# Optimization experiments

Hardware: AMD Instinct MI355X
Metric: run time of the kernel (lower is better)

## Reference

```python
import jax, jax.numpy as jnp
import numpy as np

EPS = 1e-5

def _layernorm(x, g, b):
    mu = jnp.mean(x, axis=-1, keepdims=True)
    var = jnp.mean((x - mu) ** 2, axis=-1, keepdims=True)
    return (x - mu) / jnp.sqrt(var + EPS) * g + b


def setup_inputs() -> dict:
    key = jax.random.key(0)
    ks = jax.random.split(key, 4)
    B, H, W, C = 8, 96, 96, 256
    return {
        "x1": jax.random.normal(ks[0], (B, H, W, C), dtype=jnp.float32),
        "x2": jax.random.normal(ks[1], (B, H, W, C), dtype=jnp.float32),
        # norm1 (shared LayerNorm applied to both x1 and x2)
        "g1": jnp.ones((C,), jnp.float32),
        "b1": jnp.zeros((C,), jnp.float32),
        # reprojection 1x1 conv: C -> 2C
        "Wr": jax.random.normal(ks[2], (2 * C, C), dtype=jnp.float32) * 0.05,
        "br": jnp.zeros((2 * C,), jnp.float32),
        # final LayerNorm over 2C
        "g2": jnp.ones((2 * C,), jnp.float32),
        "b2": jnp.zeros((2 * C,), jnp.float32),
        # learnable mixing scalars
        "a1": jnp.array(0.25, jnp.float32),
        "a2": jnp.array(0.25, jnp.float32),
        "a3": jnp.array(0.25, jnp.float32),
        "a4": jnp.array(0.25, jnpp_ := jnp.float32),
    }


def reference(x1, x2, g1, b1, Wr, br, g2, b2, a1, a2, a3, a4):
    B, H, W, C = x1.shape
    N, D = H * W, C  # head_count = 1, key_channels = value_channels = D
    n1 = _layernorm(x1.reshape(B, N, C), g1, b1)  # [B,N,D]
    n2 = _layernorm(x2.reshape(B, N, C), g1, b1)

    kq = jnp.swapaxes(n2, 1, 2)                   # [B,D,N]
    key_sm = jax.nn.softmax(kq, axis=2)           # softmax over N
    query = jax.nn.softmax(kq, axis=1)            # softmax over D
    value = jnp.swapaxes(n1, 1, 2)                # [B,D,N]

    # context = key @ value^T : [B,D,D]
    context = jnp.einsum('bdn,ben->bde', key_sm, value)

    def masked_softmax(k):
        # torch.topk + scatter mask == keep entries >= k-th largest per row
        thr = jax.lax.top_k(context, k)[0][..., -1:]
        return jax.nn.softmax(jnp.where(context >= thr, context, -jnp.inf), axis=-1)

    ks = [D // 2, (D * 2) // 3, (D * 3) // 4, (D * 4) // 5]
    o = [jnp.einsum('bde,ben->bdn', masked_softmax(k), query) for k in ks]
    att = a1 * o[0] + a2 * o[1] + a3 * o[2] + a4 * o[3]  # [B,D,N]

    # 1x1 conv reprojection D -> 2D, then LayerNorm over channels
    rep = jnp.einsum('oc,bcn->bno', Wr, att) + br         # [B,N,2D]
    rep = _layernorm(rep, g2, b2)
    # view(B,H,W,2C).permute(0,3,1,2)
    return jnp.transpose(rep.reshape(B, H, W, 2 * C), (0, 3, 1, 2))
```

## Files before the change

### kernel.cpp

```cpp
#include <hip/hip_runtime.h>
#include <hip/hip_bf16.h>

#define Bc 8
#define Nn 9216
#define Dd 256
#define Oo 512
#define EPSc 1e-5f

#define OFF_MU1    0
#define OFF_RSTD1  73728
#define OFF_MU2    147456
#define OFF_RSTD2  221184
#define OFF_ROWINV 294912
#define OFF_COLSUM 368640
#define OFF_M      894976
#define OFF_W2T    1419264
#define OFF_CTXP   2467840

typedef __attribute__((ext_vector_type(4))) float f32x4;
typedef __attribute__((ext_vector_type(8))) short short8;
typedef __attribute__((ext_vector_type(8))) unsigned short ushort8;

static __device__ __forceinline__ unsigned short f2bf(float f) {
    __hip_bfloat16 h = __float2bfloat16(f);
    union { __hip_bfloat16 hh; unsigned short uu; } cv; cv.hh = h;
    return cv.uu;
}

#define SWZ(ch) (((((ch) >> 2) & 7)) ^ ((((ch) & 3)) << 1))

__global__ __launch_bounds__(256) void mg_k0_zero(float* __restrict__ p, int n4) {
    int i = blockIdx.x * 256 + threadIdx.x;
    if (i < n4) ((float4*)p)[i] = make_float4(0.f, 0.f, 0.f, 0.f);
}

__global__ __launch_bounds__(256) void mg_k1_stats(const float* __restrict__ x1, const float* __restrict__ x2,
                                                   const float* __restrict__ g1, const float* __restrict__ b1,
                                                   float* __restrict__ ws)
{
    float* mu1    = ws + OFF_MU1;
    float* rstd1  = ws + OFF_RSTD1;
    float* mu2    = ws + OFF_MU2;
    float* rstd2  = ws + OFF_RSTD2;
    float* rowinv = ws + OFF_ROWINV;
    float* colsum = ws + OFF_COLSUM;

    int t = threadIdx.x, lane = t & 63, w = t >> 6;
    int b = blockIdx.x / 144, rb = blockIdx.x % 144;
    int nbase = rb * 64;

    float4 g1v = ((const float4*)g1)[lane];
    float4 b1v = ((const float4*)b1)[lane];
    float cs0 = 0.f, cs1 = 0.f, cs2 = 0.f, cs3 = 0.f;
    __shared__ float csL[4][256];

    for (int i = 0; i < 16; ++i) {
        int n = nbase + i * 4 + w;
        int base = (b * Nn + n) * 64 + lane;
        float4 xa = ((const float4*)x1)[base];
        float4 xb = ((const float4*)x2)[base];
        float s1 = xa.x + xa.y + xa.z + xa.w;
        float q1 = xa.x*xa.x + xa.y*xa.y + xa.z*xa.z + xa.w*xa.w;
        float s2 = xb.x + xb.y + xb.z + xb.w;
        float q2 = xb.x*xb.x + xb.y*xb.y + xb.z*xb.z + xb.w*xb.w;
        #pragma unroll
        for (int m = 1; m < 64; m <<= 1) {
            s1 += __shfl_xor(s1, m); q1 += __shfl_xor(q1, m);
            s2 += __shfl_xor(s2, m); q2 += __shfl_xor(q2, m);
        }
        float m1 = s1 * (1.f / Dd), m2 = s2 * (1.f / Dd);
        float r1 = rsqrtf(q1 * (1.f / Dd) - m1 * m1 + EPSc);
        float r2 = rsqrtf(q2 * (1.f / Dd) - m2 * m2 + EPSc);
        int ni = b * Nn + n;
        if (lane == 0) { mu1[ni] = m1; rstd1[ni] = r1; mu2[ni] = m2; rstd2[ni] = r2; }
        float e0 = __expf((xb.x - m2) * r2 * g1v.x + b1v.x);
        float e1 = __expf((xb.y - m2) * r2 * g1v.y + b1v.y);
        float e2 = __expf((xb.z - m2) * r2 * g1v.z + b1v.z);
        float e3 = __expf((xb.w - m2) * r2 * g1v.w + b1v.w);
        float rs = e0 + e1 + e2 + e3;
        #pragma unroll
        for (int m = 1; m < 64; m <<= 1) rs += __shfl_xor(rs, m);
        if (lane == 0) rowinv[ni] = 1.f / rs;
        cs0 += e0; cs1 += e1; cs2 += e2; cs3 += e3;
    }
    csL[w][lane * 4 + 0] = cs0;
    csL[w][lane * 4 + 1] = cs1;
    csL[w][lane * 4 + 2] = cs2;
    csL[w][lane * 4 + 3] = cs3;
    __syncthreads();
    float tot = csL[0][t] + csL[1][t] + csL[2][t] + csL[3][t];
    atomicAdd(&colsum[b * Dd + t], tot);
}

__global__ __launch_bounds__(512, 2) void mg_k3_ctx(const float* __restrict__ x1, const float* __restrict__ x2,
                                                    const float* __restrict__ g1, const float* __restrict__ b1,
                                                    float* __restrict__ ws, int nks)
{
    __shared__ ushort PA[256 * 64];
    __shared__ ushort PB[256 * 64];
    const float* mu1   = ws + OFF_MU1;
    const float* rstd1 = ws + OFF_RSTD1;
    const float* mu2   = ws + OFF_MU2;
    const float* rstd2 = ws + OFF_RSTD2;
    float* ctxp = ws + OFF_CTXP;

    int t = threadIdx.x;
    int ks_i = blockIdx.x % nks;
    int b = blockIdx.x / nks;
    int krange = Nn / nks;
    int ntiles = krange >> 6;
    int n_base = ks_i * krange;

    int o  = t >> 6;
    int c4 = t & 63;

    f32x4 g1v = ((const f32x4*)g1)[c4];
    f32x4 b1v = ((const f32x4*)b1)[c4];

    int lane = t & 63, wave = t >> 6;
    int wd = wave & 3, we = wave >> 2;
    int l15 = lane & 15, kgrp = lane >> 4;

    f32x4 acc[4][8];
    #pragma unroll
    for (int dt = 0; dt < 4; ++dt)
        #pragma unroll
        for (int et = 0; et < 8; ++et) acc[dt][et] = (f32x4){0.f, 0.f, 0.f, 0.f};

    for (int st = 0; st < ntiles; ++st) {
        int rowb = b * Nn + n_base + st * 64 + o * 8;
        __syncthreads();
        {
            f32x4 mv0 = *(const f32x4*)(mu1 + rowb),   mv1 = *(const f32x4*)(mu1 + rowb + 4);
            f32x4 rv0 = *(const f32x4*)(rstd1 + rowb), rv1 = *(const f32x4*)(rstd1 + rowb + 4);
            float mva[8] = {mv0[0], mv0[1], mv0[2], mv0[3], mv1[0], mv1[1], mv1[2], mv1[3]};
            float rva[8] = {rv0[0], rv0[1], rv0[2], rv0[3], rv1[0], rv1[1], rv1[2], rv1[3]};
            f32x4 xv[8];
            #pragma unroll
            for (int rr = 0; rr < 8; ++rr)
                xv[rr] = ((const f32x4*)x1)[(size_t)(rowb + rr) * 64 + c4];
            #pragma unroll
            for (int i = 0; i < 4; ++i) {
                int ch = c4 * 4 + i;
                ushort8 u;
                #pragma unroll
                for (int rr = 0; rr < 8; ++rr)
                    u[rr] = f2bf((xv[rr][i] - mva[rr]) * rva[rr] * g1v[i] + b1v[i]);
                *(ushort8*)&PB[ch * 64 + ((o + SWZ(ch)) & 7) * 8] = u;
            }
        }
        {
            f32x4 mv0 = *(const f32x4*)(mu2 + rowb),   mv1 = *(const f32x4*)(mu2 + rowb + 4);
            f32x4 rv0 = *(const f32x4*)(rstd2 + rowb), rv1 = *(const f32x4*)(rstd2 + rowb + 4);
            float mva[8] = {mv0[0], mv0[1], mv0[2], mv0[3], mv1[0], mv1[1], mv1[2], mv1[3]};
            float rva[8] = {rv0[0], rv0[1], rv0[2], rv0[3], rv1[0], rv1[1], rv1[2], rv1[3]};
            f32x4 xv[8];
            #pragma unroll
            for (int rr = 0; rr < 8; ++rr)
                xv[rr] = ((const f32x4*)x2)[(size_t)(rowb + rr) * 64 + c4];
            #pragma unroll
            for (int i = 0; i < 4; ++i) {
                int ch = c4 * 4 + i;
                ushort8 u;
                #pragma unroll
                for (int rr = 0; rr < 8; ++rr)
                    u[rr] = f2bf(__expf((xv[rr][i] - mva[rr]) * rva[rr] * g1v[i] + b1v[i]));
                *(ushort8*)&PA[ch * 64 + ((o + SWZ(ch)) & 7) * 8] = u;
            }
        }
        __syncthreads();

        #pragma unroll
        for (int kk = 0; kk < 2; ++kk) {
            short8 af[4], bf[8];
            #pragma unroll
            for (int dt = 0; dt < 4; ++dt) {
                int ch = wd * 64 + dt * 16 + l15;
                af[dt] = *(const short8*)&PA[ch * 64 + (((kk << 2) + kgrp + SWZ(ch)) & 7) * 8];
            }
            #pragma unroll
            for (int et = 0; et < 8; ++et) {
                int ch = we * 128 + et * 16 + l15;
                bf[et] = *(const short8*)&PB[ch * 64 + (((kk << 2) + kgrp + SWZ(ch)) & 7) * 8];
            }
            #pragma unroll
            for (int dt = 0; dt < 4; ++dt)
                #pragma unroll
                for (int et = 0; et < 8; ++et)
                    acc[dt][et] = __builtin_amdgcn_mfma_f32_16x16x32_bf16(af[dt], bf[et], acc[dt][et], 0, 0, 0);
        }
    }

    size_t obase = ((size_t)ks_i * Bc + b) * (Dd * Dd);
    #pragma unroll
    for (int dt = 0; dt < 4; ++dt) {
        #pragma unroll
        for (int r = 0; r < 4; ++r) {
            int d = wd * 64 + dt * 16 + kgrp * 4 + r;
            float* rowp = ctxp + obase + (size_t)d * Dd + we * 128 + l15;
            #pragma unroll
            for (int et = 0; et < 8; ++et)
                rowp[et * 16] = acc[dt][et][r];
        }
    }
}

__global__ __launch_bounds__(256) void mg_k5_mask(const float* __restrict__ a1p, const float* __restrict__ a2p,
                                                  const float* __restrict__ a3p, const float* __restrict__ a4p,
                                                  float* __restrict__ ws, int nks)
{
    const float* ctxp   = ws + OFF_CTXP;
    const float* colsum = ws + OFF_COLSUM;
    float* Mo = ws + OFF_M;
    int t = threadIdx.x;
    int b = blockIdx.x >> 8, d = blockIdx.x & 255;
    __shared__ float s[256];
    __shared__ float wred[4][4];

    float c = 0.f;
    for (int p = 0; p < nks; ++p)
        c += ctxp[((size_t)p * Bc + b) * (Dd * Dd) + (size_t)d * Dd + t];
    float inv = 1.f / colsum[b * Dd + d];
    c *= inv;
    s[t] = c;
    __syncthreads();
    for (int k = 2; k <= 256; k <<= 1) {
        for (int j = k >> 1; j > 0; j >>= 1) {
            int ixj = t ^ j;
            if (ixj > t) {
                float A = s[t], Bv = s[ixj];
                bool desc = ((t & k) == 0);
                bool sw = desc ? (A < Bv) : (A > Bv);
                if (sw) { s[t] = Bv; s[ixj] = A; }
            }
            __syncthreads();
        }
    }
    float cmax = s[0];
    float t0 = s[127], t1 = s[169], t2 = s[191], t3 = s[203];
    float e = __expf(c - cmax);
    float w0 = (c >= t0) ? e : 0.f;
    float w1 = (c >= t1) ? e : 0.f;
    float w2 = (c >= t2) ? e : 0.f;
    float w3 = (c >= t3) ? e : 0.f;
    float v0 = w0, v1 = w1, v2 = w2, v3 = w3;
    #pragma unroll
    for (int m = 1; m < 64; m <<= 1) {
        v0 += __shfl_xor(v0, m); v1 += __shfl_xor(v1, m);
        v2 += __shfl_xor(v2, m); v3 += __shfl_xor(v3, m);
    }
    int lane = t & 63, wv = t >> 6;
    if (lane == 0) { wred[wv][0] = v0; wred[wv][1] = v1; wred[wv][2] = v2; wred[wv][3] = v3; }
    __syncthreads();
    float S0 = wred[0][0] + wred[1][0] + wred[2][0] + wred[3][0];
    float S1 = wred[0][1] + wred[1][1] + wred[2][1] + wred[3][1];
    float S2 = wred[0][2] + wred[1][2] + wred[2][2] + wred[3][2];
    float S3 = wred[0][3] + wred[1][3] + wred[2][3] + wred[3][3];
    float Mv = a1p[0] * (w0 / S0) + a2p[0] * (w1 / S1) + a3p[0] * (w2 / S2) + a4p[0] * (w3 / S3);
    Mo[(b * Dd + d) * Dd + t] = Mv;
}

__global__ __launch_bounds__(256) void mg_k6_w2(const float* __restrict__ Wr, float* __restrict__ ws)
{
    const float* Mo = ws + OFF_M;
    ushort* W2B = (ushort*)(ws + OFF_W2T);
    __shared__ float Mt[32][128];
    __shared__ float WrT[32][36];
    int t = threadIdx.x;
    int b = blockIdx.x >> 5, ob = (blockIdx.x >> 1) & 15, eh = blockIdx.x & 1;
    int o0 = ob * 32, e0 = eh * 128;
    int ol4 = t & 7, el = t >> 3;
    float acc[4][4];
    #pragma unroll
    for (int i = 0; i < 4; ++i)
        #pragma unroll
        for (int j = 0; j < 4; ++j) acc[i][j] = 0.f;

    for (int ch = 0; ch < 8; ++ch) {
        int c0 = ch * 32;
        __syncthreads();
        #pragma unroll
        for (int k = 0; k < 4; ++k) {
            int fi = t + k * 256;
            int row = fi >> 5, c4 = fi & 31;
            float4 mv = ((const float4*)Mo)[(b * Dd + c0 + row) * 64 + (e0 >> 2) + c4];
            *(float4*)&Mt[row][c4 * 4] = mv;
        }
        {
            int ol = t >> 3, c4 = t & 7;
            float4 wv = ((const float4*)Wr)[(o0 + ol) * 64 + (c0 >> 2) + c4];
            WrT[c4 * 4 + 0][ol] = wv.x;
            WrT[c4 * 4 + 1][ol] = wv.y;
            WrT[c4 * 4 + 2][ol] = wv.z;
            WrT[c4 * 4 + 3][ol] = wv.w;
        }
        __syncthreads();
        #pragma unroll
        for (int cc = 0; cc < 32; ++cc) {
            float4 w4 = *(const float4*)&WrT[cc][ol4 * 4];
            float4 m4 = *(const float4*)&Mt[cc][el * 4];
            float wv[4] = {w4.x, w4.y, w4.z, w4.w};
            float mv[4] = {m4.x, m4.y, m4.z, m4.w};
            #pragma unroll
            for (int i = 0; i < 4; ++i)
                #pragma unroll
                for (int j = 0; j < 4; ++j)
                    acc[i][j] = fmaf(wv[i], mv[j], acc[i][j]);
        }
    }
    {
        int ee = e0 + el * 4;
        int ks = ee >> 5, eloc = ee & 31;
        #pragma unroll
        for (int i = 0; i < 4; ++i) {
            int o = o0 + ol4 * 4 + i;
            ushort4 u;
            u.x = f2bf(acc[i][0]); u.y = f2bf(acc[i][1]);
            u.z = f2bf(acc[i][2]); u.w = f2bf(acc[i][3]);
            *(ushort4*)&W2B[(((size_t)b * 8 + ks) * Oo + o) * 32 + eloc] = u;
        }
    }
}

__global__ __launch_bounds__(512) void mg_k7_final(const float* __restrict__ x2,
        const float* __restrict__ g1, const float* __restrict__ b1,
        const float* __restrict__ br, const float* __restrict__ g2, const float* __restrict__ b2,
        const float* __restrict__ ws, float* __restrict__ out)
{
    __shared__ ushort qsT[32 * 256];
    __shared__ float stat[8][2][16][2];
    __shared__ float musig[32][2];

    const float* mu2    = ws + OFF_MU2;
    const float* rstd2  = ws + OFF_RSTD2;
    const float* rowinv = ws + OFF_ROWINV;
    const ushort* W2B   = (const ushort*)(ws + OFF_W2T);

    int t = threadIdx.x;
    int b = blockIdx.x / 288, nt0 = blockIdx.x % 288;
    int n0 = nt0 * 32;

    {
        int row = t >> 4, gb = (t & 15) * 2;
        int ni = b * Nn + n0 + row;
        float m = mu2[ni], r = rstd2[ni], ri = rowinv[ni];
        #pragma unroll
        for (int jj = 0; jj < 2; ++jj) {
            int g = gb + jj;
            const float4* xp = (const float4*)x2 + (size_t)ni * 64 + g * 2;
            float4 xa = xp[0], xb = xp[1];
            float4 ga = ((const float4*)g1)[g * 2], gc = ((const float4*)g1)[g * 2 + 1];
            float4 ba = ((const float4*)b1)[g * 2], bc = ((const float4*)b1)[g * 2 + 1];
            float v[8]  = {xa.x, xa.y, xa.z, xa.w, xb.x, xb.y, xb.z, xb.w};
            float gv[8] = {ga.x, ga.y, ga.z, ga.w, gc.x, gc.y, gc.z, gc.w};
            float bv[8] = {ba.x, ba.y, ba.z, ba.w, bc.x, bc.y, bc.z, bc.w};
            ushort8 u;
            #pragma unroll
            for (int q = 0; q < 8; ++q)
                u[q] = f2bf(__expf((v[q] - m) * r * gv[q] + bv[q]) * ri);
            *(ushort8*)&qsT[row * 256 + ((g ^ (row & 7)) << 3)] = u;
        }
    }
    __syncthreads();

    int lw = t & 63, wave = t >> 6;
    int colA = lw & 15, kgrp = lw >> 4;

    f32x4 acc[4][2];
    #pragma unroll
    for (int ot = 0; ot < 4; ++ot) {
        acc[ot][0] = (f32x4){0.f, 0.f, 0.f, 0.f};
        acc[ot][1] = (f32x4){0.f, 0.f, 0.f, 0.f};
    }

    const ushort* abase = W2B + ((size_t)b * 8 * Oo + wave * 64 + colA) * 32 + kgrp * 8;

#define LOADAF(dst, ksv)                                                         \
    {                                                                            \
        _Pragma("unroll")                                                        \
        for (int ot = 0; ot < 4; ++ot)                                           \
            dst[ot] = *(const short8*)&abase[((size_t)(ksv) * Oo + ot * 16) * 32];\
    }

#define MFMASTEP(afv, ksv)                                                       \
    {                                                                            \
        int gsl = (((ksv) * 4 + kgrp) ^ (colA & 7)) << 3;                        \
        short8 bf0 = *(const short8*)&qsT[colA * 256 + gsl];                     \
        short8 bf1 = *(const short8*)&qsT[(16 + colA) * 256 + gsl];              \
        _Pragma("unroll")                                                        \
        for (int ot = 0; ot < 4; ++ot) {                                         \
            acc[ot][0] = __builtin_amdgcn_mfma_f32_16x16x32_bf16(                \
                afv[ot], bf0, acc[ot][0], 0, 0, 0);                              \
            acc[ot][1] = __builtin_amdgcn_mfma_f32_16x16x32_bf16(                \
                afv[ot], bf1, acc[ot][1], 0, 0, 0);                              \
        }                                                                        \
    }

    short8 afA[4], afB[4];
    LOADAF(afA, 0);
    #pragma unroll
    for (int kp = 0; kp < 4; ++kp) {
        LOADAF(afB, 2 * kp + 1);
        MFMASTEP(afA, 2 * kp);
        if (kp < 3) LOADAF(afA, 2 * kp + 2);
        MFMASTEP(afB, 2 * kp + 1);
    }
#undef LOADAF
#undef MFMASTEP

    float ps[2] = {0.f, 0.f}, pq[2] = {0.f, 0.f};
    #pragma unroll
    for (int ot = 0; ot < 4; ++ot) {
        #pragma unroll
        for (int r = 0; r < 4; ++r) {
            int o = wave * 64 + ot * 16 + kgrp * 4 + r;
            float bb = br[o];
            float v0 = acc[ot][0][r] + bb;
            float v1 = acc[ot][1][r] + bb;
            acc[ot][0][r] = v0; acc[ot][1][r] = v1;
            ps[0] += v0; pq[0] += v0 * v0;
            ps[1] += v1; pq[1] += v1 * v1;
        }
    }
    #pragma unroll
    for (int m = 16; m <= 32; m <<= 1) {
        ps[0] += __shfl_xor(ps[0], m); pq[0] += __shfl_xor(pq[0], m);
        ps[1] += __shfl_xor(ps[1], m); pq[1] += __shfl_xor(pq[1], m);
    }
    if (lw < 16) {
        stat[wave][0][lw][0] = ps[0]; stat[wave][0][lw][1] = pq[0];
        stat[wave][1][lw][0] = ps[1]; stat[wave][1][lw][1] = pq[1];
    }
    __syncthreads();
    if (t < 32) {
        int ntl = t >> 4, col = t & 15;
        float S = 0.f, Q = 0.f;
        #pragma unroll
        for (int w2 = 0; w2 < 8; ++w2) { S += stat[w2][ntl][col][0]; Q += stat[w2][ntl][col][1]; }
        float mu = S * (1.f / Oo);
        float var = Q * (1.f / Oo) - mu * mu;
        musig[t][0] = mu;
        musig[t][1] = rsqrtf(var + EPSc);
    }
    __syncthreads();

    float mn0 = musig[colA][0],      rs0 = musig[colA][1];
    float mn1 = musig[16 + colA][0], rs1 = musig[16 + colA][1];
    #pragma unroll
    for (int ot = 0; ot < 4; ++ot) {
        #pragma unroll
        for (int r = 0; r < 4; ++r) {
            int o = wave * 64 + ot * 16 + kgrp * 4 + r;
            float gg = g2[o], bb2 = b2[o];
            size_t ob = ((size_t)b * Oo + o) * Nn + n0;
            out[ob + colA]      = (acc[ot][0][r] - mn0) * rs0 * gg + bb2;
            out[ob + 16 + colA] = (acc[ot][1][r] - mn1) * rs1 * gg + bb2;
        }
    }
}

extern "C" void kernel_launch(void* const* d_in, const int* in_sizes, int n_in,
                              void* d_out, int out_size, void* d_ws, size_t ws_size,
                              hipStream_t stream)
{
    (void)in_sizes; (void)n_in; (void)out_size;
    const float* x1 = (const float*)d_in[0];
    const float* x2 = (const float*)d_in[1];
    const float* g1 = (const float*)d_in[2];
    const float* b1 = (const float*)d_in[3];
    const float* Wr = (const float*)d_in[4];
    const float* br = (const float*)d_in[5];
    const float* g2 = (const float*)d_in[6];
    const float* b2 = (const float*)d_in[7];
    const float* a1 = (const float*)d_in[8];
    const float* a2 = (const float*)d_in[9];
    const float* a3 = (const float*)d_in[10];
    const float* a4 = (const float*)d_in[11];
    float* ws = (float*)d_ws;
    float* out = (float*)d_out;

    const int cand[6] = {24, 16, 12, 8, 4, 2};
    int nks = 2;
    for (int ci = 0; ci < 6; ++ci) {
        if ((2467840ull + (size_t)cand[ci] * 524288ull) * 4ull <= ws_size) { nks = cand[ci]; break; }
    }

    hipLaunchKernelGGL(mg_k0_zero, dim3(2), dim3(256), 0, stream, ws + OFF_COLSUM, 512);
    hipLaunchKernelGGL(mg_k1_stats, dim3(1152), dim3(256), 0, stream, x1, x2, g1, b1, ws);
    hipLaunchKernelGGL(mg_k3_ctx, dim3(Bc * nks), dim3(512), 0, stream, x1, x2, g1, b1, ws, nks);
    hipLaunchKernelGGL(mg_k5_mask, dim3(2048), dim3(256), 0, stream, a1, a2, a3, a4, ws, nks);
    hipLaunchKernelGGL(mg_k6_w2, dim3(256), dim3(256), 0, stream, Wr, ws);
    hipLaunchKernelGGL(mg_k7_final, dim3(2304), dim3(512), 0, stream, x2, g1, b1, br, g2, b2, ws, out);
}
```

Before: 200.9 us.

## Fuse LayerNorm stats into the context kernel and cache bf16 query softmax

Drops the separate stats kernel. The context kernel now computes per-row LayerNorm mean and rstd, the row softmax sums and the column-sum partials itself, using wave shuffles and then an LDS reduction with an atomic add. That kernel also writes the softmax-over-D query as bf16 into a workspace buffer. The final kernel reads that buffer instead of reloading x2 and recomputing the exponentials. This removes a full extra pass over x1 and x2, and the fp32 re-read of x2, at the cost of more shuffle and exp work inside the small-grid context kernel and a larger workspace that may lower the chosen split count.

```diff
diff --git a/kernel.cpp b/kernel.cpp
--- a/kernel.cpp
+++ b/kernel.cpp
@@ -7,15 +7,11 @@
 #define Oo 512
 #define EPSc 1e-5f
 
-#define OFF_MU1    0
-#define OFF_RSTD1  73728
-#define OFF_MU2    147456
-#define OFF_RSTD2  221184
-#define OFF_ROWINV 294912
-#define OFF_COLSUM 368640
-#define OFF_M      894976
-#define OFF_W2T    1419264
-#define OFF_CTXP   2467840
+#define OFF_COLSUM 0
+#define OFF_M      2048
+#define OFF_W2T    526336
+#define OFF_QB     1050624
+#define OFF_CTXP   10487808
 
 typedef __attribute__((ext_vector_type(4))) float f32x4;
 typedef __attribute__((ext_vector_type(8))) short short8;
@@ -32,64 +28,6 @@
 __global__ __launch_bounds__(256) void mg_k0_zero(float* __restrict__ p, int n4) {
     int i = blockIdx.x * 256 + threadIdx.x;
     if (i < n4) ((float4*)p)[i] = make_float4(0.f, 0.f, 0.f, 0.f);
-}
-
-__global__ __launch_bounds__(256) void mg_k1_stats(const float* __restrict__ x1, const float* __restrict__ x2,
-                                                   const float* __restrict__ g1, const float* __restrict__ b1,
-                                                   float* __restrict__ ws)
-{
-    float* mu1    = ws + OFF_MU1;
-    float* rstd1  = ws + OFF_RSTD1;
-    float* mu2    = ws + OFF_MU2;
-    float* rstd2  = ws + OFF_RSTD2;
-    float* rowinv = ws + OFF_ROWINV;
-    float* colsum = ws + OFF_COLSUM;
-
-    int t = threadIdx.x, lane = t & 63, w = t >> 6;
-    int b = blockIdx.x / 144, rb = blockIdx.x % 144;
-    int nbase = rb * 64;
-
-    float4 g1v = ((const float4*)g1)[lane];
-    float4 b1v = ((const float4*)b1)[lane];
-    float cs0 = 0.f, cs1 = 0.f, cs2 = 0.f, cs3 = 0.f;
-    __shared__ float csL[4][256];
-
-    for (int i = 0; i < 16; ++i) {
-        int n = nbase + i * 4 + w;
-        int base = (b * Nn + n) * 64 + lane;
-        float4 xa = ((const float4*)x1)[base];
-        float4 xb = ((const float4*)x2)[base];
-        float s1 = xa.x + xa.y + xa.z + xa.w;
-        float q1 = xa.x*xa.x + xa.y*xa.y + xa.z*xa.z + xa.w*xa.w;
-        float s2 = xb.x + xb.y + xb.z + xb.w;
-        float q2 = xb.x*xb.x + xb.y*xb.y + xb.z*xb.z + xb.w*xb.w;
-        #pragma unroll
-        for (int m = 1; m < 64; m <<= 1) {
-            s1 += __shfl_xor(s1, m); q1 += __shfl_xor(q1, m);
-            s2 += __shfl_xor(s2, m); q2 += __shfl_xor(q2, m);
-        }
-        float m1 = s1 * (1.f / Dd), m2 = s2 * (1.f / Dd);
-        float r1 = rsqrtf(q1 * (1.f / Dd) - m1 * m1 + EPSc);
-        float r2 = rsqrtf(q2 * (1.f / Dd) - m2 * m2 + EPSc);
-        int ni = b * Nn + n;
-        if (lane == 0) { mu1[ni] = m1; rstd1[ni] = r1; mu2[ni] = m2; rstd2[ni] = r2; }
-        float e0 = __expf((xb.x - m2) * r2 * g1v.x + b1v.x);
-        float e1 = __expf((xb.y - m2) * r2 * g1v.y + b1v.y);
-        float e2 = __expf((xb.z - m2) * r2 * g1v.z + b1v.z);
-        float e3 = __expf((xb.w - m2) * r2 * g1v.w + b1v.w);
-        float rs = e0 + e1 + e2 + e3;
-        #pragma unroll
-        for (int m = 1; m < 64; m <<= 1) rs += __shfl_xor(rs, m);
-        if (lane == 0) rowinv[ni] = 1.f / rs;
-        cs0 += e0; cs1 += e1; cs2 += e2; cs3 += e3;
-    }
-    csL[w][lane * 4 + 0] = cs0;
-    csL[w][lane * 4 + 1] = cs1;
-    csL[w][lane * 4 + 2] = cs2;
-    csL[w][lane * 4 + 3] = cs3;
-    __syncthreads();
-    float tot = csL[0][t] + csL[1][t] + csL[2][t] + csL[3][t];
-    atomicAdd(&colsum[b * Dd + t], tot);
 }
 
 __global__ __launch_bounds__(512, 2) void mg_k3_ctx(const float* __restrict__ x1, const float* __restrict__ x2,
@@ -98,10 +36,9 @@
 {
     __shared__ ushort PA[256 * 64];
     __shared__ ushort PB[256 * 64];
-    const float* mu1   = ws + OFF_MU1;
-    const float* rstd1 = ws + OFF_RSTD1;
-    const float* mu2   = ws + OFF_MU2;
-    const float* rstd2 = ws + OFF_RSTD2;
+    __shared__ float csL[8][256];
+    float* colsum = ws + OFF_COLSUM;
+    ushort* qb = (ushort*)(ws + OFF_QB);
     float* ctxp = ws + OFF_CTXP;
 
     int t = threadIdx.x;
@@ -121,6 +58,8 @@
     int wd = wave & 3, we = wave >> 2;
     int l15 = lane & 15, kgrp = lane >> 4;
 
+    float cs[4] = {0.f, 0.f, 0.f, 0.f};
+
     f32x4 acc[4][8];
     #pragma unroll
     for (int dt = 0; dt < 4; ++dt)
@@ -131,14 +70,31 @@
         int rowb = b * Nn + n_base + st * 64 + o * 8;
         __syncthreads();
         {
-            f32x4 mv0 = *(const f32x4*)(mu1 + rowb),   mv1 = *(const f32x4*)(mu1 + rowb + 4);
-            f32x4 rv0 = *(const f32x4*)(rstd1 + rowb), rv1 = *(const f32x4*)(rstd1 + rowb + 4);
-            float mva[8] = {mv0[0], mv0[1], mv0[2], mv0[3], mv1[0], mv1[1], mv1[2], mv1[3]};
-            float rva[8] = {rv0[0], rv0[1], rv0[2], rv0[3], rv1[0], rv1[1], rv1[2], rv1[3]};
             f32x4 xv[8];
             #pragma unroll
             for (int rr = 0; rr < 8; ++rr)
                 xv[rr] = ((const f32x4*)x1)[(size_t)(rowb + rr) * 64 + c4];
+            float sA[8], qA[8];
+            #pragma unroll
+            for (int rr = 0; rr < 8; ++rr) {
+                f32x4 v = xv[rr];
+                sA[rr] = v[0] + v[1] + v[2] + v[3];
+                qA[rr] = v[0]*v[0] + v[1]*v[1] + v[2]*v[2] + v[3]*v[3];
+            }
+            #pragma unroll
+            for (int m = 1; m < 64; m <<= 1)
+                #pragma unroll
+                for (int rr = 0; rr < 8; ++rr) {
+                    sA[rr] += __shfl_xor(sA[rr], m);
+                    qA[rr] += __shfl_xor(qA[rr], m);
+                }
+            float mva[8], rva[8];
+            #pragma unroll
+            for (int rr = 0; rr < 8; ++rr) {
+                float mu = sA[rr] * (1.f / Dd);
+                mva[rr] = mu;
+                rva[rr] = rsqrtf(qA[rr] * (1.f / Dd) - mu * mu + EPSc);
+            }
             #pragma unroll
             for (int i = 0; i < 4; ++i) {
                 int ch = c4 * 4 + i;
@@ -150,22 +106,66 @@
             }
         }
         {
-            f32x4 mv0 = *(const f32x4*)(mu2 + rowb),   mv1 = *(const f32x4*)(mu2 + rowb + 4);
-            f32x4 rv0 = *(const f32x4*)(rstd2 + rowb), rv1 = *(const f32x4*)(rstd2 + rowb + 4);
-            float mva[8] = {mv0[0], mv0[1], mv0[2], mv0[3], mv1[0], mv1[1], mv1[2], mv1[3]};
-            float rva[8] = {rv0[0], rv0[1], rv0[2], rv0[3], rv1[0], rv1[1], rv1[2], rv1[3]};
             f32x4 xv[8];
             #pragma unroll
             for (int rr = 0; rr < 8; ++rr)
                 xv[rr] = ((const f32x4*)x2)[(size_t)(rowb + rr) * 64 + c4];
+            float sA[8], qA[8];
+            #pragma unroll
+            for (int rr = 0; rr < 8; ++rr) {
+                f32x4 v = xv[rr];
+                sA[rr] = v[0] + v[1] + v[2] + v[3];
+                qA[rr] = v[0]*v[0] + v[1]*v[1] + v[2]*v[2] + v[3]*v[3];
+            }
+            #pragma unroll
+            for (int m = 1; m < 64; m <<= 1)
+                #pragma unroll
+                for (int rr = 0; rr < 8; ++rr) {
+                    sA[rr] += __shfl_xor(sA[rr], m);
+                    qA[rr] += __shfl_xor(qA[rr], m);
+                }
+            float mva[8], rva[8];
+            #pragma unroll
+            for (int rr = 0; rr < 8; ++rr) {
+                float mu = sA[rr] * (1.f / Dd);
+                mva[rr] = mu;
+                rva[rr] = rsqrtf(qA[rr] * (1.f / Dd) - mu * mu + EPSc);
+            }
+            float ev[4][8];
+            #pragma unroll
+            for (int i = 0; i < 4; ++i)
+                #pragma unroll
+                for (int rr = 0; rr < 8; ++rr)
+                    ev[i][rr] = __expf((xv[rr][i] - mva[rr]) * rva[rr] * g1v[i] + b1v[i]);
+            float rsum[8];
+            #pragma unroll
+            for (int rr = 0; rr < 8; ++rr)
+                rsum[rr] = ev[0][rr] + ev[1][rr] + ev[2][rr] + ev[3][rr];
+            #pragma unroll
+            for (int m = 1; m < 64; m <<= 1)
+                #pragma unroll
+                for (int rr = 0; rr < 8; ++rr)
+                    rsum[rr] += __shfl_xor(rsum[rr], m);
             #pragma unroll
             for (int i = 0; i < 4; ++i) {
                 int ch = c4 * 4 + i;
                 ushort8 u;
                 #pragma unroll
-                for (int rr = 0; rr < 8; ++rr)
-                    u[rr] = f2bf(__expf((xv[rr][i] - mva[rr]) * rva[rr] * g1v[i] + b1v[i]));
+                for (int rr = 0; rr < 8; ++rr) {
+                    u[rr] = f2bf(ev[i][rr]);
+                    cs[i] += ev[i][rr];
+                }
                 *(ushort8*)&PA[ch * 64 + ((o + SWZ(ch)) & 7) * 8] = u;
+            }
+            #pragma unroll
+            for (int rr = 0; rr < 8; ++rr) {
+                float ri = 1.f / rsum[rr];
+                ushort4 uq;
+                uq.x = f2bf(ev[0][rr] * ri);
+                uq.y = f2bf(ev[1][rr] * ri);
+                uq.z = f2bf(ev[2][rr] * ri);
+                uq.w = f2bf(ev[3][rr] * ri);
+                *(ushort4*)&qb[(size_t)(rowb + rr) * 256 + c4 * 4] = uq;
             }
         }
         __syncthreads();
@@ -189,6 +189,16 @@
                 for (int et = 0; et < 8; ++et)
                     acc[dt][et] = __builtin_amdgcn_mfma_f32_16x16x32_bf16(af[dt], bf[et], acc[dt][et], 0, 0, 0);
         }
+    }
+
+    #pragma unroll
+    for (int i = 0; i < 4; ++i) csL[wave][c4 * 4 + i] = cs[i];
+    __syncthreads();
+    if (t < 256) {
+        float s = 0.f;
+        #pragma unroll
+        for (int w2 = 0; w2 < 8; ++w2) s += csL[w2][t];
+        atomicAdd(&colsum[b * Dd + t], s);
     }
 
     size_t obase = ((size_t)ks_i * Bc + b) * (Dd * Dd);
@@ -322,8 +332,7 @@
     }
 }
 
-__global__ __launch_bounds__(512) void mg_k7_final(const float* __restrict__ x2,
-        const float* __restrict__ g1, const float* __restrict__ b1,
+__global__ __launch_bounds__(512) void mg_k7_final(
         const float* __restrict__ br, const float* __restrict__ g2, const float* __restrict__ b2,
         const float* __restrict__ ws, float* __restrict__ out)
 {
@@ -331,33 +340,20 @@
     __shared__ float stat[8][2][16][2];
     __shared__ float musig[32][2];
 
-    const float* mu2    = ws + OFF_MU2;
-    const float* rstd2  = ws + OFF_RSTD2;
-    const float* rowinv = ws + OFF_ROWINV;
-    const ushort* W2B   = (const ushort*)(ws + OFF_W2T);
+    const ushort* qb  = (const ushort*)(ws + OFF_QB);
+    const ushort* W2B = (const ushort*)(ws + OFF_W2T);
 
     int t = threadIdx.x;
     int b = blockIdx.x / 288, nt0 = blockIdx.x % 288;
     int n0 = nt0 * 32;
 
     {
-        int row = t >> 4, gb = (t & 15) * 2;
-        int ni = b * Nn + n0 + row;
-        float m = mu2[ni], r = rstd2[ni], ri = rowinv[ni];
+        int row = t >> 4, gpair = (t & 15) * 2;
+        size_t ni = (size_t)(b * Nn + n0 + row);
         #pragma unroll
         for (int jj = 0; jj < 2; ++jj) {
-            int g = gb + jj;
-            const float4* xp = (const float4*)x2 + (size_t)ni * 64 + g * 2;
-            float4 xa = xp[0], xb = xp[1];
-            float4 ga = ((const float4*)g1)[g * 2], gc = ((const float4*)g1)[g * 2 + 1];
-            float4 ba = ((const float4*)b1)[g * 2], bc = ((const float4*)b1)[g * 2 + 1];
-            float v[8]  = {xa.x, xa.y, xa.z, xa.w, xb.x, xb.y, xb.z, xb.w};
-            float gv[8] = {ga.x, ga.y, ga.z, ga.w, gc.x, gc.y, gc.z, gc.w};
-            float bv[8] = {ba.x, ba.y, ba.z, ba.w, bc.x, bc.y, bc.z, bc.w};
-            ushort8 u;
-            #pragma unroll
-            for (int q = 0; q < 8; ++q)
-                u[q] = f2bf(__expf((v[q] - m) * r * gv[q] + bv[q]) * ri);
+            int g = gpair + jj;
+            ushort8 u = *(const ushort8*)&qb[ni * 256 + g * 8];
             *(ushort8*)&qsT[row * 256 + ((g ^ (row & 7)) << 3)] = u;
         }
     }
@@ -482,13 +478,12 @@
     const int cand[6] = {24, 16, 12, 8, 4, 2};
     int nks = 2;
     for (int ci = 0; ci < 6; ++ci) {
-        if ((2467840ull + (size_t)cand[ci] * 524288ull) * 4ull <= ws_size) { nks = cand[ci]; break; }
+        if (((size_t)OFF_CTXP + (size_t)cand[ci] * 524288ull) * 4ull <= ws_size) { nks = cand[ci]; break; }
     }
 
     hipLaunchKernelGGL(mg_k0_zero, dim3(2), dim3(256), 0, stream, ws + OFF_COLSUM, 512);
-    hipLaunchKernelGGL(mg_k1_stats, dim3(1152), dim3(256), 0, stream, x1, x2, g1, b1, ws);
     hipLaunchKernelGGL(mg_k3_ctx, dim3(Bc * nks), dim3(512), 0, stream, x1, x2, g1, b1, ws, nks);
     hipLaunchKernelGGL(mg_k5_mask, dim3(2048), dim3(256), 0, stream, a1, a2, a3, a4, ws, nks);
     hipLaunchKernelGGL(mg_k6_w2, dim3(256), dim3(256), 0, stream, Wr, ws);
-    hipLaunchKernelGGL(mg_k7_final, dim3(2304), dim3(512), 0, stream, x2, g1, b1, br, g2, b2, ws, out);
-}
+    hipLaunchKernelGGL(mg_k7_final, dim3(2304), dim3(512), 0, stream, br, g2, b2, ws, out);
+}
```

Measured after the change: 239.5 us. 19.2% more time.

## Precompute bf16 query softmax in stats kernel and double-buffer final GEMM tiles

Applied to the files above, without the earlier changes.

The stats kernel now writes the normalized softmax-over-channels query as bf16 to workspace, so the final kernel no longer rereads x2 in fp32 or recomputes the exponentials. The final kernel processes three 32-column tiles per block, loading each tile into one of two LDS buffers while it computes on the other. This removes redundant exp work and cuts the final kernel's input traffic. In exchange it adds a bf16 write of the query in the stats kernel, a larger workspace, and fewer, longer blocks.

```diff
diff --git a/kernel.cpp b/kernel.cpp
--- a/kernel.cpp
+++ b/kernel.cpp
@@ -11,11 +11,11 @@
 #define OFF_RSTD1  73728
 #define OFF_MU2    147456
 #define OFF_RSTD2  221184
-#define OFF_ROWINV 294912
-#define OFF_COLSUM 368640
-#define OFF_M      894976
-#define OFF_W2T    1419264
-#define OFF_CTXP   2467840
+#define OFF_COLSUM 294912
+#define OFF_M      296960
+#define OFF_W2T    821248
+#define OFF_QB     1345536
+#define OFF_CTXP   10782720
 
 typedef __attribute__((ext_vector_type(4))) float f32x4;
 typedef __attribute__((ext_vector_type(8))) short short8;
@@ -42,8 +42,8 @@
     float* rstd1  = ws + OFF_RSTD1;
     float* mu2    = ws + OFF_MU2;
     float* rstd2  = ws + OFF_RSTD2;
-    float* rowinv = ws + OFF_ROWINV;
     float* colsum = ws + OFF_COLSUM;
+    ushort* qb    = (ushort*)(ws + OFF_QB);
 
     int t = threadIdx.x, lane = t & 63, w = t >> 6;
     int b = blockIdx.x / 144, rb = blockIdx.x % 144;
@@ -80,7 +80,11 @@
         float rs = e0 + e1 + e2 + e3;
         #pragma unroll
         for (int m = 1; m < 64; m <<= 1) rs += __shfl_xor(rs, m);
-        if (lane == 0) rowinv[ni] = 1.f / rs;
+        float ri = 1.f / rs;
+        ushort4 uq;
+        uq.x = f2bf(e0 * ri); uq.y = f2bf(e1 * ri);
+        uq.z = f2bf(e2 * ri); uq.w = f2bf(e3 * ri);
+        *(ushort4*)&qb[(size_t)ni * 256 + lane * 4] = uq;
         cs0 += e0; cs1 += e1; cs2 += e2; cs3 += e3;
     }
     csL[w][lane * 4 + 0] = cs0;
@@ -322,58 +326,36 @@
     }
 }
 
-__global__ __launch_bounds__(512) void mg_k7_final(const float* __restrict__ x2,
-        const float* __restrict__ g1, const float* __restrict__ b1,
+__global__ __launch_bounds__(512) void mg_k7_final(
         const float* __restrict__ br, const float* __restrict__ g2, const float* __restrict__ b2,
         const float* __restrict__ ws, float* __restrict__ out)
 {
-    __shared__ ushort qsT[32 * 256];
+    __shared__ ushort qsT[2][32 * 256];
     __shared__ float stat[8][2][16][2];
     __shared__ float musig[32][2];
 
-    const float* mu2    = ws + OFF_MU2;
-    const float* rstd2  = ws + OFF_RSTD2;
-    const float* rowinv = ws + OFF_ROWINV;
-    const ushort* W2B   = (const ushort*)(ws + OFF_W2T);
+    const ushort* qb  = (const ushort*)(ws + OFF_QB);
+    const ushort* W2B = (const ushort*)(ws + OFF_W2T);
 
     int t = threadIdx.x;
-    int b = blockIdx.x / 288, nt0 = blockIdx.x % 288;
-    int n0 = nt0 * 32;
-
-    {
-        int row = t >> 4, gb = (t & 15) * 2;
-        int ni = b * Nn + n0 + row;
-        float m = mu2[ni], r = rstd2[ni], ri = rowinv[ni];
-        #pragma unroll
-        for (int jj = 0; jj < 2; ++jj) {
-            int g = gb + jj;
-            const float4* xp = (const float4*)x2 + (size_t)ni * 64 + g * 2;
-            float4 xa = xp[0], xb = xp[1];
-            float4 ga = ((const float4*)g1)[g * 2], gc = ((const float4*)g1)[g * 2 + 1];
-            float4 ba = ((const float4*)b1)[g * 2], bc = ((const float4*)b1)[g * 2 + 1];
-            float v[8]  = {xa.x, xa.y, xa.z, xa.w, xb.x, xb.y, xb.z, xb.w};
-            float gv[8] = {ga.x, ga.y, ga.z, ga.w, gc.x, gc.y, gc.z, gc.w};
-            float bv[8] = {ba.x, ba.y, ba.z, ba.w, bc.x, bc.y, bc.z, bc.w};
-            ushort8 u;
-            #pragma unroll
-            for (int q = 0; q < 8; ++q)
-                u[q] = f2bf(__expf((v[q] - m) * r * gv[q] + bv[q]) * ri);
-            *(ushort8*)&qsT[row * 256 + ((g ^ (row & 7)) << 3)] = u;
-        }
-    }
-    __syncthreads();
+    int b = blockIdx.x / 96, nb = blockIdx.x % 96;
 
     int lw = t & 63, wave = t >> 6;
     int colA = lw & 15, kgrp = lw >> 4;
 
-    f32x4 acc[4][2];
-    #pragma unroll
-    for (int ot = 0; ot < 4; ++ot) {
-        acc[ot][0] = (f32x4){0.f, 0.f, 0.f, 0.f};
-        acc[ot][1] = (f32x4){0.f, 0.f, 0.f, 0.f};
-    }
-
     const ushort* abase = W2B + ((size_t)b * 8 * Oo + wave * 64 + colA) * 32 + kgrp * 8;
+
+#define STAGEQ(bufv, sv)                                                        \
+    {                                                                           \
+        int row_ = t >> 4, gpair_ = (t & 15) * 2;                               \
+        size_t ni_ = (size_t)(b * Nn + (nb * 3 + (sv)) * 32 + row_);            \
+        _Pragma("unroll")                                                       \
+        for (int jj = 0; jj < 2; ++jj) {                                        \
+            int g_ = gpair_ + jj;                                               \
+            ushort8 u_ = *(const ushort8*)&qb[ni_ * 256 + g_ * 8];              \
+            *(ushort8*)&qsT[bufv][row_ * 256 + ((g_ ^ (row_ & 7)) << 3)] = u_;  \
+        }                                                                       \
+    }
 
 #define LOADAF(dst, ksv)                                                         \
     {                                                                            \
@@ -382,11 +364,11 @@
             dst[ot] = *(const short8*)&abase[((size_t)(ksv) * Oo + ot * 16) * 32];\
     }
 
-#define MFMASTEP(afv, ksv)                                                       \
+#define MFMASTEP(afv, ksv, bufv)                                                 \
     {                                                                            \
         int gsl = (((ksv) * 4 + kgrp) ^ (colA & 7)) << 3;                        \
-        short8 bf0 = *(const short8*)&qsT[colA * 256 + gsl];                     \
-        short8 bf1 = *(const short8*)&qsT[(16 + colA) * 256 + gsl];              \
+        short8 bf0 = *(const short8*)&qsT[bufv][colA * 256 + gsl];               \
+        short8 bf1 = *(const short8*)&qsT[bufv][(16 + colA) * 256 + gsl];        \
         _Pragma("unroll")                                                        \
         for (int ot = 0; ot < 4; ++ot) {                                         \
             acc[ot][0] = __builtin_amdgcn_mfma_f32_16x16x32_bf16(                \
@@ -396,67 +378,85 @@
         }                                                                        \
     }
 
-    short8 afA[4], afB[4];
-    LOADAF(afA, 0);
-    #pragma unroll
-    for (int kp = 0; kp < 4; ++kp) {
-        LOADAF(afB, 2 * kp + 1);
-        MFMASTEP(afA, 2 * kp);
-        if (kp < 3) LOADAF(afA, 2 * kp + 2);
-        MFMASTEP(afB, 2 * kp + 1);
-    }
+    STAGEQ(0, 0);
+    __syncthreads();
+    int cur = 0;
+
+    for (int s = 0; s < 3; ++s) {
+        if (s < 2) STAGEQ(cur ^ 1, s + 1);
+
+        f32x4 acc[4][2];
+        #pragma unroll
+        for (int ot = 0; ot < 4; ++ot) {
+            acc[ot][0] = (f32x4){0.f, 0.f, 0.f, 0.f};
+            acc[ot][1] = (f32x4){0.f, 0.f, 0.f, 0.f};
+        }
+
+        short8 afA[4], afB[4];
+        LOADAF(afA, 0);
+        #pragma unroll
+        for (int kp = 0; kp < 4; ++kp) {
+            LOADAF(afB, 2 * kp + 1);
+            MFMASTEP(afA, 2 * kp, cur);
+            if (kp < 3) LOADAF(afA, 2 * kp + 2);
+            MFMASTEP(afB, 2 * kp + 1, cur);
+        }
+
+        int n0 = (nb * 3 + s) * 32;
+        float ps[2] = {0.f, 0.f}, pq[2] = {0.f, 0.f};
+        #pragma unroll
+        for (int ot = 0; ot < 4; ++ot) {
+            #pragma unroll
+            for (int r = 0; r < 4; ++r) {
+                int o = wave * 64 + ot * 16 + kgrp * 4 + r;
+                float bb = br[o];
+                float v0 = acc[ot][0][r] + bb;
+                float v1 = acc[ot][1][r] + bb;
+                acc[ot][0][r] = v0; acc[ot][1][r] = v1;
+                ps[0] += v0; pq[0] += v0 * v0;
+                ps[1] += v1; pq[1] += v1 * v1;
+            }
+        }
+        #pragma unroll
+        for (int m = 16; m <= 32; m <<= 1) {
+            ps[0] += __shfl_xor(ps[0], m); pq[0] += __shfl_xor(pq[0], m);
+            ps[1] += __shfl_xor(ps[1], m); pq[1] += __shfl_xor(pq[1], m);
+        }
+        if (lw < 16) {
+            stat[wave][0][lw][0] = ps[0]; stat[wave][0][lw][1] = pq[0];
+            stat[wave][1][lw][0] = ps[1]; stat[wave][1][lw][1] = pq[1];
+        }
+        __syncthreads();
+        if (t < 32) {
+            int ntl = t >> 4, col = t & 15;
+            float S = 0.f, Q = 0.f;
+            #pragma unroll
+            for (int w2 = 0; w2 < 8; ++w2) { S += stat[w2][ntl][col][0]; Q += stat[w2][ntl][col][1]; }
+            float mu = S * (1.f / Oo);
+            float var = Q * (1.f / Oo) - mu * mu;
+            musig[t][0] = mu;
+            musig[t][1] = rsqrtf(var + EPSc);
+        }
+        __syncthreads();
+
+        float mn0 = musig[colA][0],      rs0 = musig[colA][1];
+        float mn1 = musig[16 + colA][0], rs1 = musig[16 + colA][1];
+        #pragma unroll
+        for (int ot = 0; ot < 4; ++ot) {
+            #pragma unroll
+            for (int r = 0; r < 4; ++r) {
+                int o = wave * 64 + ot * 16 + kgrp * 4 + r;
+                float gg = g2[o], bb2 = b2[o];
+                size_t ob = ((size_t)b * Oo + o) * Nn + n0;
+                out[ob + colA]      = (acc[ot][0][r] - mn0) * rs0 * gg + bb2;
+                out[ob + 16 + colA] = (acc[ot][1][r] - mn1) * rs1 * gg + bb2;
+            }
+        }
+        cur ^= 1;
+    }
+#undef STAGEQ
 #undef LOADAF
 #undef MFMASTEP
-
-    float ps[2] = {0.f, 0.f}, pq[2] = {0.f, 0.f};
-    #pragma unroll
-    for (int ot = 0; ot < 4; ++ot) {
-        #pragma unroll
-        for (int r = 0; r < 4; ++r) {
-            int o = wave * 64 + ot * 16 + kgrp * 4 + r;
-            float bb = br[o];
-            float v0 = acc[ot][0][r] + bb;
-            float v1 = acc[ot][1][r] + bb;
-            acc[ot][0][r] = v0; acc[ot][1][r] = v1;
-            ps[0] += v0; pq[0] += v0 * v0;
-            ps[1] += v1; pq[1] += v1 * v1;
-        }
-    }
-    #pragma unroll
-    for (int m = 16; m <= 32; m <<= 1) {
-        ps[0] += __shfl_xor(ps[0], m); pq[0] += __shfl_xor(pq[0], m);
-        ps[1] += __shfl_xor(ps[1], m); pq[1] += __shfl_xor(pq[1], m);
-    }
-    if (lw < 16) {
-        stat[wave][0][lw][0] = ps[0]; stat[wave][0][lw][1] = pq[0];
-        stat[wave][1][lw][0] = ps[1]; stat[wave][1][lw][1] = pq[1];
-    }
-    __syncthreads();
-    if (t < 32) {
-        int ntl = t >> 4, col = t & 15;
-        float S = 0.f, Q = 0.f;
-        #pragma unroll
-        for (int w2 = 0; w2 < 8; ++w2) { S += stat[w2][ntl][col][0]; Q += stat[w2][ntl][col][1]; }
-        float mu = S * (1.f / Oo);
-        float var = Q * (1.f / Oo) - mu * mu;
-        musig[t][0] = mu;
-        musig[t][1] = rsqrtf(var + EPSc);
-    }
-    __syncthreads();
-
-    float mn0 = musig[colA][0],      rs0 = musig[colA][1];
-    float mn1 = musig[16 + colA][0], rs1 = musig[16 + colA][1];
-    #pragma unroll
-    for (int ot = 0; ot < 4; ++ot) {
-        #pragma unroll
-        for (int r = 0; r < 4; ++r) {
-            int o = wave * 64 + ot * 16 + kgrp * 4 + r;
-            float gg = g2[o], bb2 = b2[o];
-            size_t ob = ((size_t)b * Oo + o) * Nn + n0;
-            out[ob + colA]      = (acc[ot][0][r] - mn0) * rs0 * gg + bb2;
-            out[ob + 16 + colA] = (acc[ot][1][r] - mn1) * rs1 * gg + bb2;
-        }
-    }
 }
 
 extern "C" void kernel_launch(void* const* d_in, const int* in_sizes, int n_in,
@@ -482,7 +482,7 @@
     const int cand[6] = {24, 16, 12, 8, 4, 2};
     int nks = 2;
     for (int ci = 0; ci < 6; ++ci) {
-        if ((2467840ull + (size_t)cand[ci] * 524288ull) * 4ull <= ws_size) { nks = cand[ci]; break; }
+        if (((size_t)OFF_CTXP + (size_t)cand[ci] * 524288ull) * 4ull <= ws_size) { nks = cand[ci]; break; }
     }
 
     hipLaunchKernelGGL(mg_k0_zero, dim3(2), dim3(256), 0, stream, ws + OFF_COLSUM, 512);
@@ -490,5 +490,5 @@
     hipLaunchKernelGGL(mg_k3_ctx, dim3(Bc * nks), dim3(512), 0, stream, x1, x2, g1, b1, ws, nks);
     hipLaunchKernelGGL(mg_k5_mask, dim3(2048), dim3(256), 0, stream, a1, a2, a3, a4, ws, nks);
     hipLaunchKernelGGL(mg_k6_w2, dim3(256), dim3(256), 0, stream, Wr, ws);
-    hipLaunchKernelGGL(mg_k7_final, dim3(2304), dim3(512), 0, stream, x2, g1, b1, br, g2, b2, ws, out);
-}
+    hipLaunchKernelGGL(mg_k7_final, dim3(768), dim3(512), 0, stream, br, g2, b2, ws, out);
+}
```

Result: slower. 314.3 us (+56.5%).

## Stage W2 tiles into LDS via async global_load_lds with double buffering

Applied to the files above, without the earlier changes.

Changes the W2B layout produced by mg_k6_w2 so each wave's MFMA A-fragments are contiguous, then streams each k-slice into LDS with global_load_lds, double-buffered, in mg_k7_final. LDS is reused for the stats arrays afterwards, and the workspace offsets are compacted. The goal is to hide global-load latency behind the MFMA work and the x2 normalisation. In exchange it adds a __syncthreads per k-step and uses about 80KB of LDS per block, which may lower occupancy.

```diff
diff --git a/kernel.cpp b/kernel.cpp
--- a/kernel.cpp
+++ b/kernel.cpp
@@ -13,9 +13,9 @@
 #define OFF_RSTD2  221184
 #define OFF_ROWINV 294912
 #define OFF_COLSUM 368640
-#define OFF_M      894976
-#define OFF_W2T    1419264
-#define OFF_CTXP   2467840
+#define OFF_M      370688
+#define OFF_W2T    894976
+#define OFF_CTXP   1419264
 
 typedef __attribute__((ext_vector_type(4))) float f32x4;
 typedef __attribute__((ext_vector_type(8))) short short8;
@@ -309,15 +309,19 @@
         }
     }
     {
-        int ee = e0 + el * 4;
-        int ks = ee >> 5, eloc = ee & 31;
+        int e_base = e0 + el * 4;
+        int ks = e_base >> 5;
+        int kg = (e_base >> 3) & 3, jj = e_base & 7;
         #pragma unroll
         for (int i = 0; i < 4; ++i) {
             int o = o0 + ol4 * 4 + i;
+            int wv2 = o >> 6, ot = (o >> 4) & 3, cA = o & 15;
             ushort4 u;
             u.x = f2bf(acc[i][0]); u.y = f2bf(acc[i][1]);
             u.z = f2bf(acc[i][2]); u.w = f2bf(acc[i][3]);
-            *(ushort4*)&W2B[(((size_t)b * 8 + ks) * Oo + o) * 32 + eloc] = u;
+            size_t idx = ((size_t)b * 8 + ks) * 16384 + wv2 * 2048 + ot * 512
+                       + (kg * 16 + cA) * 8 + jj;
+            *(ushort4*)&W2B[idx] = u;
         }
     }
 }
@@ -327,9 +331,10 @@
         const float* __restrict__ br, const float* __restrict__ g2, const float* __restrict__ b2,
         const float* __restrict__ ws, float* __restrict__ out)
 {
-    __shared__ ushort qsT[32 * 256];
-    __shared__ float stat[8][2][16][2];
-    __shared__ float musig[32][2];
+    __shared__ ushort smem[8192 + 2 * 16384];
+    ushort* qsT = smem;
+    ushort* W0 = smem + 8192;
+    ushort* W1 = smem + 8192 + 16384;
 
     const float* mu2    = ws + OFF_MU2;
     const float* rstd2  = ws + OFF_RSTD2;
@@ -339,14 +344,32 @@
     int t = threadIdx.x;
     int b = blockIdx.x / 288, nt0 = blockIdx.x % 288;
     int n0 = nt0 * 32;
+    int lw = t & 63, wave = t >> 6;
+    int colA = lw & 15, kgrp = lw >> 4;
+
+#define STAGEW(dstbuf, ksv)                                                        \
+    {                                                                              \
+        size_t so_ = ((size_t)b * 8 + (ksv)) * 16384 + wave * 2048;                \
+        _Pragma("unroll")                                                          \
+        for (int k_ = 0; k_ < 4; ++k_) {                                           \
+            __builtin_amdgcn_global_load_lds(                                      \
+                (const __attribute__((address_space(1))) unsigned int*)            \
+                    (W2B + so_ + k_ * 512 + lw * 8),                               \
+                (__attribute__((address_space(3))) unsigned int*)                  \
+                    ((dstbuf) + wave * 2048 + k_ * 512),                           \
+                16, 0, 0);                                                         \
+        }                                                                          \
+    }
+
+    STAGEW(W0, 0);
 
     {
-        int row = t >> 4, gb = (t & 15) * 2;
+        int row = t >> 4, gpair = (t & 15) * 2;
         int ni = b * Nn + n0 + row;
         float m = mu2[ni], r = rstd2[ni], ri = rowinv[ni];
         #pragma unroll
         for (int jj = 0; jj < 2; ++jj) {
-            int g = gb + jj;
+            int g = gpair + jj;
             const float4* xp = (const float4*)x2 + (size_t)ni * 64 + g * 2;
             float4 xa = xp[0], xb = xp[1];
             float4 ga = ((const float4*)g1)[g * 2], gc = ((const float4*)g1)[g * 2 + 1];
@@ -363,9 +386,6 @@
     }
     __syncthreads();
 
-    int lw = t & 63, wave = t >> 6;
-    int colA = lw & 15, kgrp = lw >> 4;
-
     f32x4 acc[4][2];
     #pragma unroll
     for (int ot = 0; ot < 4; ++ot) {
@@ -373,40 +393,28 @@
         acc[ot][1] = (f32x4){0.f, 0.f, 0.f, 0.f};
     }
 
-    const ushort* abase = W2B + ((size_t)b * 8 * Oo + wave * 64 + colA) * 32 + kgrp * 8;
-
-#define LOADAF(dst, ksv)                                                         \
-    {                                                                            \
-        _Pragma("unroll")                                                        \
-        for (int ot = 0; ot < 4; ++ot)                                           \
-            dst[ot] = *(const short8*)&abase[((size_t)(ksv) * Oo + ot * 16) * 32];\
-    }
-
-#define MFMASTEP(afv, ksv)                                                       \
-    {                                                                            \
-        int gsl = (((ksv) * 4 + kgrp) ^ (colA & 7)) << 3;                        \
-        short8 bf0 = *(const short8*)&qsT[colA * 256 + gsl];                     \
-        short8 bf1 = *(const short8*)&qsT[(16 + colA) * 256 + gsl];              \
-        _Pragma("unroll")                                                        \
-        for (int ot = 0; ot < 4; ++ot) {                                         \
-            acc[ot][0] = __builtin_amdgcn_mfma_f32_16x16x32_bf16(                \
-                afv[ot], bf0, acc[ot][0], 0, 0, 0);                              \
-            acc[ot][1] = __builtin_amdgcn_mfma_f32_16x16x32_bf16(                \
-                afv[ot], bf1, acc[ot][1], 0, 0, 0);                              \
-        }                                                                        \
-    }
-
-    short8 afA[4], afB[4];
-    LOADAF(afA, 0);
-    #pragma unroll
-    for (int kp = 0; kp < 4; ++kp) {
-        LOADAF(afB, 2 * kp + 1);
-        MFMASTEP(afA, 2 * kp);
-        if (kp < 3) LOADAF(afA, 2 * kp + 2);
-        MFMASTEP(afB, 2 * kp + 1);
-    }
-#undef LOADAF
-#undef MFMASTEP
+    #pragma unroll
+    for (int ks = 0; ks < 8; ++ks) {
+        if (ks < 7) {
+            if ((ks & 1) == 0) { STAGEW(W1, ks + 1); }
+            else               { STAGEW(W0, ks + 1); }
+        }
+        const ushort* wb = (ks & 1) ? W1 : W0;
+        int gsl = ((ks * 4 + kgrp) ^ (colA & 7)) << 3;
+        short8 bf0 = *(const short8*)&qsT[colA * 256 + gsl];
+        short8 bf1 = *(const short8*)&qsT[(16 + colA) * 256 + gsl];
+        #pragma unroll
+        for (int ot = 0; ot < 4; ++ot) {
+            short8 af = *(const short8*)&wb[wave * 2048 + ot * 512 + lw * 8];
+            acc[ot][0] = __builtin_amdgcn_mfma_f32_16x16x32_bf16(af, bf0, acc[ot][0], 0, 0, 0);
+            acc[ot][1] = __builtin_amdgcn_mfma_f32_16x16x32_bf16(af, bf1, acc[ot][1], 0, 0, 0);
+        }
+        __syncthreads();
+    }
+#undef STAGEW
+
+    float (*stat)[2][16][2] = (float (*)[2][16][2])(void*)smem;
+    float (*musig)[2] = (float (*)[2])((float*)(void*)smem + 512);
 
     float ps[2] = {0.f, 0.f}, pq[2] = {0.f, 0.f};
     #pragma unroll
@@ -482,7 +490,7 @@
     const int cand[6] = {24, 16, 12, 8, 4, 2};
     int nks = 2;
     for (int ci = 0; ci < 6; ++ci) {
-        if ((2467840ull + (size_t)cand[ci] * 524288ull) * 4ull <= ws_size) { nks = cand[ci]; break; }
+        if (((size_t)OFF_CTXP + (size_t)cand[ci] * 524288ull) * 4ull <= ws_size) { nks = cand[ci]; break; }
     }
 
     hipLaunchKernelGGL(mg_k0_zero, dim3(2), dim3(256), 0, stream, ws + OFF_COLSUM, 512);
```

After: 191.1 us (median of 2 runs). -4.9%, faster.
